# Optimization experiments

Hardware: AMD Instinct MI355X
Metric: run time of the kernel (lower is better)

## Reference

```python
import jax, jax.numpy as jnp
import numpy as np

N_HEAD = 16


def setup_inputs() -> dict:
    key = jax.random.key(0)
    k1, k2, k3 = jax.random.split(key, 3)
    B, T, C = 2, 2048, 1024
    x = jax.random.normal(k1, (B, T, C), dtype=jnp.float32)
    # Linear params (torch Linear: y = x @ W.T + b), scaled for stability
    w_attn = jax.random.normal(k2, (3 * C, C), dtype=jnp.float32) * (C ** -0.5)
    b_attn = jnp.zeros((3 * C,), dtype=jnp.float32)
    w_proj = jax.random.normal(k3, (C, C), dtype=jnp.float32) * (C ** -0.5)
    b_proj = jnp.zeros((C,), dtype=jnp.float32)
    return {"x": x, "w_attn": w_attn, "b_attn": b_attn,
            "w_proj": w_proj, "b_proj": b_proj}


def reference(x, w_attn, b_attn, w_proj, b_proj):
    B, T, C = x.shape
    H = N_HEAD
    hd = C // H
    # qkv projection: [B, T, 3C]
    qkv = jnp.einsum('btc,dc->btd', x, w_attn) + b_attn
    # NOTE: original views as (B, T, H, 3*hd) then splits last dim -> per-head
    # interleaved qkv layout (NOT the standard 3-way split of full projection).
    qkv = qkv.reshape(B, T, H, 3 * hd).transpose(0, 2, 1, 3)  # [B, H, T, 3*hd]
    q, k, v = qkv[..., :hd], qkv[..., hd:2 * hd], qkv[..., 2 * hd:]
    # NOTE: scale uses full embedding dim C, not head_dim (faithful to source).
    attn = jnp.einsum('bhqd,bhkd->bhqk', q, k) * (C ** -0.5)
    # NOTE: no causal mask in the original despite the class name.
    attn = jax.nn.softmax(attn, axis=-1)
    y = jnp.einsum('bhqk,bhkd->bhqd', attn, v)  # [B, H, T, hd]
    y = y.transpose(0, 2, 1, 3).reshape(B, T, C)
    y = jnp.einsum('btc,dc->btd', y, w_proj) + b_proj
    return y
```

## Files before the change

### kernel.cpp

```cpp
#include <hip/hip_runtime.h>
#include <hip/hip_bf16.h>

typedef unsigned short u16;
typedef __bf16 bf16x8 __attribute__((ext_vector_type(8)));
typedef float f32x4 __attribute__((ext_vector_type(4)));
typedef float f32x16 __attribute__((ext_vector_type(16)));
typedef unsigned u32x4 __attribute__((ext_vector_type(4)));

#define QSCALE 0.045084220027780106f

__device__ __forceinline__ u16 f2b(float f) {
  unsigned x = __float_as_uint(f);
  unsigned r = (x + 0x7fffu + ((x >> 16) & 1u)) >> 16;
  return (u16)r;
}

__device__ __forceinline__ void gll16(const void* g, void* l) {
  __builtin_amdgcn_global_load_lds((const __attribute__((address_space(1))) void*)g,
                                   (__attribute__((address_space(3))) void*)l, 16, 0, 0);
}

__device__ __forceinline__ f32x4 mfma16(bf16x8 a, bf16x8 b, f32x4 c) {
  return __builtin_amdgcn_mfma_f32_16x16x32_bf16(a, b, c, 0, 0, 0);
}
__device__ __forceinline__ f32x16 mfma32(bf16x8 a, bf16x8 b, f32x16 c) {
  return __builtin_amdgcn_mfma_f32_32x32x16_bf16(a, b, c, 0, 0, 0);
}

__device__ __forceinline__ void plswap(unsigned& a, unsigned& b) {
  asm volatile("v_permlane32_swap_b32 %0, %1" : "+v"(a), "+v"(b));
}
__device__ __forceinline__ unsigned cvtpk(float lo, float hi) {
  unsigned r;
  asm("v_cvt_pk_bf16_f32 %0, %1, %2" : "=v"(r) : "v"(lo), "v"(hi));
  return r;
}

#define WAITV(N) asm volatile("s_waitcnt vmcnt(" #N ")" ::: "memory")
#define BAR()                              \
  do {                                     \
    __builtin_amdgcn_s_barrier();          \
    __builtin_amdgcn_sched_barrier(0);     \
  } while (0)

__global__ __launch_bounds__(256) void cvt3(const float* __restrict__ x,
                                            const float* __restrict__ wa,
                                            const float* __restrict__ wp,
                                            u16* __restrict__ dx,
                                            u16* __restrict__ dwa,
                                            u16* __restrict__ dwp) {
  const int N1 = 4194304, N2 = 3145728;
  int i = (blockIdx.x * 256 + threadIdx.x) * 4;
  const float* s;
  u16* d;
  int off;
  if (i < N1) { s = x; d = dx; off = i; }
  else if (i < N1 + N2) { s = wa; d = dwa; off = i - N1; }
  else { s = wp; d = dwp; off = i - N1 - N2; }
  float4 v = *(const float4*)(s + off);
  ushort4 o;
  o.x = f2b(v.x); o.y = f2b(v.y); o.z = f2b(v.z); o.w = f2b(v.w);
  *(ushort4*)(d + off) = o;
}

__global__ __launch_bounds__(512) void gemm_qkv(const u16* __restrict__ A,
                                                const u16* __restrict__ W,
                                                const float* __restrict__ bias,
                                                u16* __restrict__ Qb,
                                                u16* __restrict__ Kb,
                                                u16* __restrict__ Vtb) {
  __shared__ u16 As[2][256 * 64];
  __shared__ u16 Bs[2][256 * 64];
  const int K = 1024;
  int o = blockIdx.x;
  int xcd = o & 7, li = o >> 3;
  int bm = (xcd >> 1) * 4 + li / 6;
  int bn = (xcd & 1) * 6 + li % 6;
  int tid = threadIdx.x, lane = tid & 63, w = tid >> 6;
  int wm = w >> 2, wn = w & 3, g = lane >> 4, c = lane & 15;
  f32x4 acc[8][4] = {};
  const u16* Arow = A + (size_t)(bm * 256) * K;
  const u16* Wrow = W + (size_t)(bn * 256) * K;

  const u16* asrc[4];
  const u16* bsrc[4];
  int sdst[4];
#pragma unroll
  for (int rr = 0; rr < 4; ++rr) {
    int ci = rr * 512 + tid;
    int row = ci >> 3, sseg = (ci & 7) ^ (row & 7);
    asrc[rr] = Arow + (size_t)row * K + sseg * 8;
    bsrc[rr] = Wrow + (size_t)row * K + sseg * 8;
    sdst[rr] = ci * 8;
  }
  auto stage = [&](int buf) {
#pragma unroll
    for (int rr = 0; rr < 4; ++rr) gll16(asrc[rr], &As[buf][sdst[rr]]);
#pragma unroll
    for (int rr = 0; rr < 4; ++rr) gll16(bsrc[rr], &Bs[buf][sdst[rr]]);
#pragma unroll
    for (int rr = 0; rr < 4; ++rr) { asrc[rr] += 64; bsrc[rr] += 64; }
  };

  stage(0);
  int cur = 0;
  for (int k0 = 0; k0 < K; k0 += 64) {
    __syncthreads();
    if (k0 + 64 < K) stage(cur ^ 1);
#pragma unroll
    for (int kk = 0; kk < 2; ++kk) {
      bf16x8 af[8], bfr[4];
#pragma unroll
      for (int mi = 0; mi < 8; ++mi) {
        int row = wm * 128 + mi * 16 + c;
        af[mi] = *(const bf16x8*)&As[cur][row * 64 + (((kk * 4 + g) ^ (row & 7)) * 8)];
      }
#pragma unroll
      for (int ni = 0; ni < 4; ++ni) {
        int row = wn * 64 + ni * 16 + c;
        bfr[ni] = *(const bf16x8*)&Bs[cur][row * 64 + (((kk * 4 + g) ^ (row & 7)) * 8)];
      }
      __builtin_amdgcn_s_setprio(1);
#pragma unroll
      for (int mi = 0; mi < 8; ++mi)
#pragma unroll
        for (int ni = 0; ni < 4; ++ni)
          acc[mi][ni] = mfma16(af[mi], bfr[ni], acc[mi][ni]);
      __builtin_amdgcn_s_setprio(0);
    }
    cur ^= 1;
  }

  __syncthreads();
  u16* VT = &As[0][0];
  int bb = bm >> 3;
  int tbase = (bm & 7) << 8;
  int m = (bn * 64) % 192;
  int base_h = (bn * 256) / 192;

  int cls[4], qkoff[4], vb[4], vx[4];
  float bi[4];
#pragma unroll
  for (int ni = 0; ni < 4; ++ni) {
    int cl = wn * 64 + ni * 16 + c;
    bi[ni] = bias[bn * 256 + cl];
    int q = cl + m;
    int rh = q >= 192;
    int j = q - rh * 192;
    int bh = bb * 16 + base_h + rh;
    if (j < 64) { cls[ni] = 0; qkoff[ni] = bh * 131072 + j; }
    else if (j < 128) { cls[ni] = 1; qkoff[ni] = bh * 131072 + (j - 64); }
    else { cls[ni] = 2; int vcl = rh * 64 + (j - 128); vb[ni] = vcl * 256; vx[ni] = (vcl & 15) << 3; }
  }
#pragma unroll
  for (int mi = 0; mi < 8; ++mi)
#pragma unroll
    for (int r = 0; r < 4; ++r) {
      int trow = wm * 128 + mi * 16 + g * 4 + r;
      int t = tbase + trow;
#pragma unroll
      for (int ni = 0; ni < 4; ++ni) {
        float v = acc[mi][ni][r] + bi[ni];
        if (cls[ni] == 0) Qb[(size_t)qkoff[ni] + t * 64] = f2b(v * QSCALE);
        else if (cls[ni] == 1) Kb[(size_t)qkoff[ni] + t * 64] = f2b(v);
        else VT[vb[ni] + (trow ^ vx[ni])] = f2b(v);
      }
    }
  __syncthreads();
  int nV = (m == 128) ? 128 : 64;
  for (int id = tid; id < nV * 32; id += 512) {
    int vcl = id >> 5, tc = id & 31;
    bf16x8 vv = *(const bf16x8*)&VT[vcl * 256 + ((tc * 8) ^ ((vcl & 15) << 3))];
    int rh = vcl >> 6, d = vcl & 63;
    size_t dst = ((size_t)(bb * 16 + base_h + rh) * 64 + d) * 2048 + tbase + tc * 8;
    *(bf16x8*)&Vtb[dst] = vv;
  }
}

__global__ __launch_bounds__(256, 4) void attn_kernel(const u16* __restrict__ Qb,
                                                      const u16* __restrict__ Kb,
                                                      const u16* __restrict__ Vtb,
                                                      u16* __restrict__ Yb) {
  __shared__ u16 SMEM[2][2][2][2048];
  int bh = blockIdx.y;
  int b = bh >> 4, hh = bh & 15;
  int tid = threadIdx.x, lane = tid & 63, wv = tid >> 6;
  int wq = wv & 1, wk = wv >> 1;
  int c5 = lane & 31, h = lane >> 5;
  int q0 = blockIdx.x * 64 + wq * 32;
  const u16* Qh = Qb + (size_t)bh * 2048 * 64;
  const u16* Kh = Kb + (size_t)bh * 2048 * 64;
  const u16* Vh = Vtb + (size_t)bh * 64 * 2048;

  const u16* Qrow = Qh + (size_t)(q0 + c5) * 64;
  bf16x8 qf[4];
#pragma unroll
  for (int dc = 0; dc < 4; ++dc)
    qf[dc] = *(const bf16x8*)&Qrow[dc * 16 + h * 8];

  f32x16 acc0 = {}, acc1 = {};
  float mx = -1e30f, ls = 0.f;

  const u16* gsrc[4];
  int gstep[4];
  u16* ld0[4];
  u16* ld1[4];
#pragma unroll
  for (int part = 0; part < 4; ++part) {
    int ci = part * 256 + tid;
    int st = ci >> 9;
    int rem = ci & 511;
    int kv = rem >> 8;
    int slot = rem & 255;
    int row = slot >> 3, seg = slot & 7;
    int sseg = seg ^ (row & 7);
    int t0 = st * 1024;
    if (kv == 0) {
      gsrc[part] = Kh + (size_t)(t0 + row) * 64 + sseg * 8;
      gstep[part] = 32 * 64;
    } else {
      int dh = sseg >> 2, ksl = sseg & 3;
      gsrc[part] = Vh + (size_t)(dh * 32 + row) * 2048 + t0 + ksl * 8;
      gstep[part] = 32;
    }
    ld0[part] = &SMEM[st][0][kv][slot * 8];
    ld1[part] = &SMEM[st][1][kv][slot * 8];
  }
  auto stagepair = [&](int buf) {
#pragma unroll
    for (int part = 0; part < 4; ++part) {
      gll16(gsrc[part], buf ? ld1[part] : ld0[part]);
      gsrc[part] += gstep[part];
    }
  };

  stagepair(0);
  int cur = 0;
  for (int it = 0; it < 32; ++it) {
    __syncthreads();
    if (it + 1 < 32) stagepair(cur ^ 1);
    const u16* Kt = &SMEM[wk][cur][0][0];
    const u16* Vt = &SMEM[wk][cur][1][0];

    f32x16 s0 = {};
    __builtin_amdgcn_s_setprio(1);
#pragma unroll
    for (int dc = 0; dc < 4; ++dc) {
      bf16x8 kf = *(const bf16x8*)&Kt[c5 * 64 + (((dc * 2 + h) ^ (c5 & 7)) * 8)];
      s0 = mfma32(kf, qf[dc], s0);
    }
    __builtin_amdgcn_s_setprio(0);

    float t4[4];
#pragma unroll
    for (int i = 0; i < 4; ++i)
      t4[i] = fmaxf(fmaxf(s0[i], s0[i + 4]), fmaxf(s0[i + 8], s0[i + 12]));
    float mtile = fmaxf(fmaxf(t4[0], t4[1]), fmaxf(t4[2], t4[3]));
    mtile = fmaxf(mtile, __shfl_xor(mtile, 32));
    if (!__all(mtile - mx <= 8.0f)) {
      float mn = fmaxf(mx, mtile);
      float corr = exp2f(mx - mn);
      ls *= corr;
      mx = mn;
#pragma unroll
      for (int j = 0; j < 16; ++j) {
        float cb = __shfl(corr, (j & 3) + 8 * (j >> 2) + 4 * h, 64);
        acc0[j] *= cb;
        acc1[j] *= cb;
      }
    }
#pragma unroll
    for (int j = 0; j < 16; ++j) s0[j] = exp2f(s0[j] - mx);
#pragma unroll
    for (int i = 0; i < 4; ++i)
      t4[i] = (s0[i] + s0[i + 4]) + (s0[i + 8] + s0[i + 12]);
    ls += (t4[0] + t4[1]) + (t4[2] + t4[3]);

    unsigned w0[8];
#pragma unroll
    for (int q2 = 0; q2 < 4; ++q2)
#pragma unroll
      for (int pp = 0; pp < 2; ++pp)
        w0[q2 * 2 + pp] = cvtpk(s0[q2 * 4 + 2 * pp], s0[q2 * 4 + 2 * pp + 1]);

    __builtin_amdgcn_s_setprio(1);
#pragma unroll
    for (int ks2 = 0; ks2 < 2; ++ks2) {
      unsigned a0 = w0[4 * ks2 + 0], b0 = w0[4 * ks2 + 2];
      unsigned a1 = w0[4 * ks2 + 1], b1 = w0[4 * ks2 + 3];
      plswap(a0, b0);
      plswap(a1, b1);
      u32x4 aw = {a0, a1, b0, b1};
      bf16x8 af = __builtin_bit_cast(bf16x8, aw);
      bf16x8 vf0 = *(const bf16x8*)&Vt[c5 * 64 + (((ks2 * 2 + h) ^ (c5 & 7)) * 8)];
      bf16x8 vf1 = *(const bf16x8*)&Vt[c5 * 64 + (((4 + ks2 * 2 + h) ^ (c5 & 7)) * 8)];
      acc0 = mfma32(af, vf0, acc0);
      acc1 = mfma32(af, vf1, acc1);
    }
    __builtin_amdgcn_s_setprio(0);
    cur ^= 1;
  }

  float* MG = (float*)&SMEM[0][0][0][0];
  int gi = wq * 64 + lane;
  __syncthreads();
  if (wk == 1) {
    MG[gi] = mx;
    MG[128 + gi] = ls;
#pragma unroll
    for (int j = 0; j < 16; ++j) {
      MG[256 + gi * 33 + j] = acc0[j];
      MG[256 + gi * 33 + 16 + j] = acc1[j];
    }
  }
  __syncthreads();
  if (wk == 0) {
    float mxB = MG[gi], lsB = MG[128 + gi];
    float m = fmaxf(mx, mxB);
    float cA = exp2f(mx - m), cB = exp2f(mxB - m);
    float l2 = ls * cA + lsB * cB;
    l2 += __shfl_xor(l2, 32);
    float inv = 1.0f / l2;
#pragma unroll
    for (int j = 0; j < 16; ++j) {
      int q = (j & 3) + 8 * (j >> 2) + 4 * h;
      float cAq = __shfl(cA, q, 64);
      float cBq = __shfl(cB, q, 64);
      float ibq = __shfl(inv, q, 64);
      float y0 = (acc0[j] * cAq + MG[256 + gi * 33 + j] * cBq) * ibq;
      float y1 = (acc1[j] * cAq + MG[256 + gi * 33 + 16 + j] * cBq) * ibq;
      int trow = q0 + q;
      size_t base = ((size_t)b * 2048 + trow) * 1024 + hh * 64;
      Yb[base + c5] = f2b(y0);
      Yb[base + 32 + c5] = f2b(y1);
    }
  }
}

__global__ __launch_bounds__(512) void gemm_proj(const u16* __restrict__ A,
                                                 const u16* __restrict__ W,
                                                 const float* __restrict__ bias,
                                                 float* __restrict__ out) {
  __shared__ u16 As[4][128 * 64];
  __shared__ u16 Bs[4][128 * 64];
  const int K = 1024;
  int o = blockIdx.x;
  int bn = o & 7, bm = o >> 3;
  int tid = threadIdx.x, lane = tid & 63, w = tid >> 6;
  int wm = w >> 1, wn = w & 1, g = lane >> 4, c = lane & 15;
  f32x4 acc[2][4] = {};
  const u16* Arow = A + (size_t)(bm * 128) * K;
  const u16* Wrow = W + (size_t)(bn * 128) * K;

  const u16* asrc[2];
  const u16* bsrc[2];
  int sdst[2];
#pragma unroll
  for (int rr = 0; rr < 2; ++rr) {
    int ci = rr * 512 + tid;
    int row = ci >> 3, sseg = (ci & 7) ^ (row & 7);
    asrc[rr] = Arow + (size_t)row * K + sseg * 8;
    bsrc[rr] = Wrow + (size_t)row * K + sseg * 8;
    sdst[rr] = ci * 8;
  }
  auto stage = [&](int step) {
    int slot = step & 3;
#pragma unroll
    for (int rr = 0; rr < 2; ++rr) gll16(asrc[rr], &As[slot][sdst[rr]]);
#pragma unroll
    for (int rr = 0; rr < 2; ++rr) gll16(bsrc[rr], &Bs[slot][sdst[rr]]);
#pragma unroll
    for (int rr = 0; rr < 2; ++rr) { asrc[rr] += 64; bsrc[rr] += 64; }
  };

  auto compute = [&](int step) {
    int slot = step & 3;
#pragma unroll
    for (int kk = 0; kk < 2; ++kk) {
      int q = kk * 4 + g;
      bf16x8 af[2], bfr[4];
#pragma unroll
      for (int mi = 0; mi < 2; ++mi) {
        int row = wm * 32 + mi * 16 + c;
        af[mi] = *(const bf16x8*)&As[slot][row * 64 + ((q ^ (row & 7)) * 8)];
      }
#pragma unroll
      for (int ni = 0; ni < 4; ++ni) {
        int row = wn * 64 + ni * 16 + c;
        bfr[ni] = *(const bf16x8*)&Bs[slot][row * 64 + ((q ^ (row & 7)) * 8)];
      }
#pragma unroll
      for (int mi = 0; mi < 2; ++mi)
#pragma unroll
        for (int ni = 0; ni < 4; ++ni)
          acc[mi][ni] = mfma16(af[mi], bfr[ni], acc[mi][ni]);
    }
  };

  stage(0);
  stage(1);
  stage(2);
  for (int t = 0; t <= 13; ++t) {
    WAITV(8);
    BAR();
    if (t <= 12) stage(t + 3);
    compute(t);
  }
  WAITV(4);
  BAR();
  compute(14);
  WAITV(0);
  BAR();
  compute(15);

#pragma unroll
  for (int mi = 0; mi < 2; ++mi)
#pragma unroll
    for (int ni = 0; ni < 4; ++ni)
#pragma unroll
      for (int r = 0; r < 4; ++r) {
        int row = bm * 128 + wm * 32 + mi * 16 + g * 4 + r;
        int col = bn * 128 + wn * 64 + ni * 16 + c;
        out[(size_t)row * 1024 + col] = acc[mi][ni][r] + bias[col];
      }
}

extern "C" void kernel_launch(void* const* d_in, const int* in_sizes, int n_in,
                              void* d_out, int out_size, void* d_ws, size_t ws_size,
                              hipStream_t stream) {
  const float* x      = (const float*)d_in[0];
  const float* w_attn = (const float*)d_in[1];
  const float* b_attn = (const float*)d_in[2];
  const float* w_proj = (const float*)d_in[3];
  const float* b_proj = (const float*)d_in[4];
  float* out = (float*)d_out;

  u16* ws = (u16*)d_ws;
  const size_t XB  = 0;
  const size_t WAB = XB + 4194304;
  const size_t WPB = WAB + 3145728;
  const size_t QB  = WPB + 1048576;
  const size_t KB  = QB + 4194304;
  const size_t VTB = KB + 4194304;
  const size_t YB  = VTB + 4194304;

  cvt3<<<8192, 256, 0, stream>>>(x, w_attn, w_proj, ws + XB, ws + WAB, ws + WPB);

  gemm_qkv<<<192, 512, 0, stream>>>(ws + XB, ws + WAB, b_attn,
                                    ws + QB, ws + KB, ws + VTB);

  attn_kernel<<<dim3(32, 32), 256, 0, stream>>>(ws + QB, ws + KB, ws + VTB, ws + YB);

  gemm_proj<<<256, 512, 0, stream>>>(ws + YB, ws + WPB, b_proj, out);
}
```

Before: 137.6 us.

## Retile QKV GEMM to 256x192 head-aligned tiles with 256 blocks and vmcnt pipelining

Changes the QKV GEMM tile width from 256 to 192 columns so each block covers exactly one head's q/k/v slice, and raises the grid from 192 to 256 blocks so every CU gets work. This simplifies the epilogue because no block straddles two heads. The main loop is restructured to issue the next stage's loads first, then wait with a vmcnt count and a barrier, with a trailing barrier after compute. The trade-off is less reuse per block, since each A tile now feeds only 192 output columns instead of 256.

```diff
diff --git a/kernel.cpp b/kernel.cpp
--- a/kernel.cpp
+++ b/kernel.cpp
@@ -70,87 +70,96 @@
                                                 u16* __restrict__ Kb,
                                                 u16* __restrict__ Vtb) {
   __shared__ u16 As[2][256 * 64];
-  __shared__ u16 Bs[2][256 * 64];
+  __shared__ u16 Bs[2][192 * 64];
   const int K = 1024;
   int o = blockIdx.x;
   int xcd = o & 7, li = o >> 3;
-  int bm = (xcd >> 1) * 4 + li / 6;
-  int bn = (xcd & 1) * 6 + li % 6;
+  int bm = (xcd >> 1) * 4 + (li >> 3);
+  int bn = (xcd & 1) * 8 + (li & 7);
   int tid = threadIdx.x, lane = tid & 63, w = tid >> 6;
   int wm = w >> 2, wn = w & 3, g = lane >> 4, c = lane & 15;
-  f32x4 acc[8][4] = {};
+  f32x4 acc[8][3] = {};
   const u16* Arow = A + (size_t)(bm * 256) * K;
-  const u16* Wrow = W + (size_t)(bn * 256) * K;
+  const u16* Wrow = W + (size_t)(bn * 192) * K;
 
   const u16* asrc[4];
-  const u16* bsrc[4];
-  int sdst[4];
+  const u16* bsrc[3];
+  int adst[4], bdst[3];
 #pragma unroll
   for (int rr = 0; rr < 4; ++rr) {
     int ci = rr * 512 + tid;
     int row = ci >> 3, sseg = (ci & 7) ^ (row & 7);
     asrc[rr] = Arow + (size_t)row * K + sseg * 8;
+    adst[rr] = ci * 8;
+  }
+#pragma unroll
+  for (int rr = 0; rr < 3; ++rr) {
+    int ci = rr * 512 + tid;
+    int row = ci >> 3, sseg = (ci & 7) ^ (row & 7);
     bsrc[rr] = Wrow + (size_t)row * K + sseg * 8;
-    sdst[rr] = ci * 8;
+    bdst[rr] = ci * 8;
   }
   auto stage = [&](int buf) {
 #pragma unroll
-    for (int rr = 0; rr < 4; ++rr) gll16(asrc[rr], &As[buf][sdst[rr]]);
-#pragma unroll
-    for (int rr = 0; rr < 4; ++rr) gll16(bsrc[rr], &Bs[buf][sdst[rr]]);
-#pragma unroll
-    for (int rr = 0; rr < 4; ++rr) { asrc[rr] += 64; bsrc[rr] += 64; }
+    for (int rr = 0; rr < 4; ++rr) gll16(asrc[rr], &As[buf][adst[rr]]);
+#pragma unroll
+    for (int rr = 0; rr < 3; ++rr) gll16(bsrc[rr], &Bs[buf][bdst[rr]]);
+#pragma unroll
+    for (int rr = 0; rr < 4; ++rr) asrc[rr] += 64;
+#pragma unroll
+    for (int rr = 0; rr < 3; ++rr) bsrc[rr] += 64;
   };
 
   stage(0);
-  int cur = 0;
-  for (int k0 = 0; k0 < K; k0 += 64) {
-    __syncthreads();
-    if (k0 + 64 < K) stage(cur ^ 1);
+  for (int t = 0; t < 16; ++t) {
+    int cur = t & 1;
+    if (t < 15) {
+      stage(cur ^ 1);
+      WAITV(7);
+    } else {
+      WAITV(0);
+    }
+    BAR();
 #pragma unroll
     for (int kk = 0; kk < 2; ++kk) {
-      bf16x8 af[8], bfr[4];
+      int q = kk * 4 + g;
+      bf16x8 af[8], bfr[3];
 #pragma unroll
       for (int mi = 0; mi < 8; ++mi) {
         int row = wm * 128 + mi * 16 + c;
-        af[mi] = *(const bf16x8*)&As[cur][row * 64 + (((kk * 4 + g) ^ (row & 7)) * 8)];
-      }
-#pragma unroll
-      for (int ni = 0; ni < 4; ++ni) {
-        int row = wn * 64 + ni * 16 + c;
-        bfr[ni] = *(const bf16x8*)&Bs[cur][row * 64 + (((kk * 4 + g) ^ (row & 7)) * 8)];
+        af[mi] = *(const bf16x8*)&As[cur][row * 64 + ((q ^ (row & 7)) * 8)];
+      }
+#pragma unroll
+      for (int ni = 0; ni < 3; ++ni) {
+        int row = wn * 48 + ni * 16 + c;
+        bfr[ni] = *(const bf16x8*)&Bs[cur][row * 64 + ((q ^ (row & 7)) * 8)];
       }
       __builtin_amdgcn_s_setprio(1);
 #pragma unroll
       for (int mi = 0; mi < 8; ++mi)
 #pragma unroll
-        for (int ni = 0; ni < 4; ++ni)
+        for (int ni = 0; ni < 3; ++ni)
           acc[mi][ni] = mfma16(af[mi], bfr[ni], acc[mi][ni]);
       __builtin_amdgcn_s_setprio(0);
     }
-    cur ^= 1;
+    BAR();
   }
 
   __syncthreads();
   u16* VT = &As[0][0];
-  int bb = bm >> 3;
+  int b = bm >> 3;
   int tbase = (bm & 7) << 8;
-  int m = (bn * 64) % 192;
-  int base_h = (bn * 256) / 192;
-
-  int cls[4], qkoff[4], vb[4], vx[4];
-  float bi[4];
-#pragma unroll
-  for (int ni = 0; ni < 4; ++ni) {
-    int cl = wn * 64 + ni * 16 + c;
-    bi[ni] = bias[bn * 256 + cl];
-    int q = cl + m;
-    int rh = q >= 192;
-    int j = q - rh * 192;
-    int bh = bb * 16 + base_h + rh;
+  int bh = b * 16 + bn;
+
+  int cls[3], qkoff[3], vb[3], vx[3];
+  float bi[3];
+#pragma unroll
+  for (int ni = 0; ni < 3; ++ni) {
+    int j = wn * 48 + ni * 16 + c;
+    bi[ni] = bias[bn * 192 + j];
     if (j < 64) { cls[ni] = 0; qkoff[ni] = bh * 131072 + j; }
     else if (j < 128) { cls[ni] = 1; qkoff[ni] = bh * 131072 + (j - 64); }
-    else { cls[ni] = 2; int vcl = rh * 64 + (j - 128); vb[ni] = vcl * 256; vx[ni] = (vcl & 15) << 3; }
+    else { cls[ni] = 2; int vcl = j - 128; vb[ni] = vcl * 256; vx[ni] = (vcl & 15) << 3; }
   }
 #pragma unroll
   for (int mi = 0; mi < 8; ++mi)
@@ -159,7 +168,7 @@
       int trow = wm * 128 + mi * 16 + g * 4 + r;
       int t = tbase + trow;
 #pragma unroll
-      for (int ni = 0; ni < 4; ++ni) {
+      for (int ni = 0; ni < 3; ++ni) {
         float v = acc[mi][ni][r] + bi[ni];
         if (cls[ni] == 0) Qb[(size_t)qkoff[ni] + t * 64] = f2b(v * QSCALE);
         else if (cls[ni] == 1) Kb[(size_t)qkoff[ni] + t * 64] = f2b(v);
@@ -167,12 +176,10 @@
       }
     }
   __syncthreads();
-  int nV = (m == 128) ? 128 : 64;
-  for (int id = tid; id < nV * 32; id += 512) {
+  for (int id = tid; id < 64 * 32; id += 512) {
     int vcl = id >> 5, tc = id & 31;
     bf16x8 vv = *(const bf16x8*)&VT[vcl * 256 + ((tc * 8) ^ ((vcl & 15) << 3))];
-    int rh = vcl >> 6, d = vcl & 63;
-    size_t dst = ((size_t)(bb * 16 + base_h + rh) * 64 + d) * 2048 + tbase + tc * 8;
+    size_t dst = ((size_t)bh * 64 + vcl) * 2048 + tbase + tc * 8;
     *(bf16x8*)&Vtb[dst] = vv;
   }
 }
@@ -446,7 +453,7 @@
 
   cvt3<<<8192, 256, 0, stream>>>(x, w_attn, w_proj, ws + XB, ws + WAB, ws + WPB);
 
-  gemm_qkv<<<192, 512, 0, stream>>>(ws + XB, ws + WAB, b_attn,
+  gemm_qkv<<<256, 512, 0, stream>>>(ws + XB, ws + WAB, b_attn,
                                     ws + QB, ws + KB, ws + VTB);
 
   attn_kernel<<<dim3(32, 32), 256, 0, stream>>>(ws + QB, ws + KB, ws + VTB, ws + YB);
```

Measured after the change: 131.1 us. 4.7% less time.
